# Performance work log

Hardware: AMD Instinct MI355X
Metric: run time of the kernel (lower is better)

The kernel has to match this reference:

```python
import jax, jax.numpy as jnp
import numpy as np

EPS = 1e-12  # VERY_SMALL_NUMBER
LN_EPS = 1e-5
N, NFEAT, NHID, A, P, HOPS = 50000, 256, 128, 32, 4, 2


def setup_inputs() -> dict:
    key = jax.random.key(0)
    ks = jax.random.split(key, 16)
    def w(i, shape, scale=0.05):
        return jax.random.normal(ks[i], shape, dtype=jnp.float32) * scale
    return {
        "x": jax.random.normal(ks[0], (N, NFEAT), dtype=jnp.float32),
        # input_mapper: Linear(nfeat,nhid) -> ReLU -> Linear(nhid,nhid)
        "im_w1": w(1, (NFEAT, NHID)), "im_b1": jnp.zeros((NHID,), jnp.float32),
        "im_w2": w(2, (NHID, NHID)),  "im_b2": jnp.zeros((NHID,), jnp.float32),
        # AnchorGraphLearner
        "anchors": w(3, (A, NHID), 1.0),
        "ml_w1": w(4, (P, 2 * NHID, NHID)), "ml_b1": jnp.zeros((P, NHID), jnp.float32),
        "ml_w2": w(5, (P, NHID)),            "ml_b2": jnp.zeros((P,), jnp.float32),
        # AnchorGNNLayer weights (xavier in torch; scaled randn here)
        "enc_w": w(6, (HOPS, NHID, NHID)), "enc_b": jnp.zeros((HOPS, NHID), jnp.float32),
        # LayerNorm
        "ln_g": jnp.ones((NHID,), jnp.float32), "ln_b": jnp.zeros((NHID,), jnp.float32),
        # classifier: Linear -> PReLU(nhid) -> Linear(nhid,2)
        "cls_w1": w(7, (NHID, NHID)), "cls_b1": jnp.zeros((NHID,), jnp.float32),
        "prelu_a": jnp.full((NHID,), 0.25, jnp.float32),
        "cls_w2": w(8, (NHID, 2)),   "cls_b2": jnp.zeros((2,), jnp.float32),
    }


def _forward(x, im_w1, im_b1, im_w2, im_b2, anchors, ml_w1, ml_b1, ml_w2, ml_b2,
             enc_w, enc_b, ln_g, ln_b, cls_w1, cls_b1, prelu_a, cls_w2, cls_b2):
    nhid = im_w2.shape[-1]
    # input_mapper (dropout is identity in eval)
    h = jnp.maximum(x @ im_w1 + im_b1, 0.0) @ im_w2 + im_b2  # [N, nhid]
    x_loc = h

    # --- AnchorGraphLearner: fused form of cat([x_i, a_j]) @ W1 ---
    Wx, Wa = ml_w1[:, :nhid, :], ml_w1[:, nhid:, :]  # each [P, nhid, nhid]
    attn = jnp.zeros((h.shape[0], anchors.shape[0]), h.dtype)
    for p in range(ml_w1.shape[0]):  # small fixed head count
        hx = h @ Wx[p]                               # [N, nhid]
        ha = anchors @ Wa[p]                         # [A, nhid]
        hid = jnp.maximum(hx[:, None, :] + ha[None, :, :] + ml_b1[p], 0.0)  # [N, A, nhid]
        attn = attn + jax.nn.sigmoid(hid @ ml_w2[p] + ml_b2[p])            # [N, A]
    adj = attn / ml_w1.shape[0]  # mean over heads, [N, A]

    # --- AnchorGNNLayer stack (anchor_mp normalized double matmul) ---
    node_norm = adj / jnp.maximum(adj.sum(axis=0, keepdims=True), EPS)     # col-normalized [N, A]
    anchor_norm = adj / jnp.maximum(adj.sum(axis=1, keepdims=True), EPS)   # row-normalized [N, A]
    xc = h
    for i in range(enc_w.shape[0]):
        support = xc @ enc_w[i]                          # [N, nhid]
        agg = node_norm.T @ support                      # [A, nhid]
        xc = jnp.maximum(anchor_norm @ agg + enc_b[i], 0.0)

    # residual + LayerNorm
    z = xc + x_loc
    mu = z.mean(axis=-1, keepdims=True)
    var = ((z - mu) ** 2).mean(axis=-1, keepdims=True)
    z = (z - mu) * jax.lax.rsqrt(var + LN_EPS) * ln_g + ln_b

    def classifier(t):
        t1 = t @ cls_w1 + cls_b1
        t1 = jnp.where(t1 > 0, t1, prelu_a * t1)  # PReLU(nhid)
        return t1 @ cls_w2 + cls_b2

    pred = classifier(z)                 # [N, 2]
    anchor_logits = classifier(anchors)  # [A, 2]
    anchor_vec = anchors[None]           # [1, A, nhid] (matches unsqueeze(0))
    return (pred, z, anchor_vec, anchor_logits)


def reference(x, im_w1, im_b1, im_w2, im_b2, anchors, ml_w1, ml_b1, ml_w2, ml_b2,
              enc_w, enc_b, ln_g, ln_b, cls_w1, cls_b1, prelu_a, cls_w2, cls_b2):
    return _forward(x, im_w1, im_b1, im_w2, im_b2, anchors, ml_w1, ml_b1, ml_w2, ml_b2,
                    enc_w, enc_b, ln_g, ln_b, cls_w1, cls_b1, prelu_a, cls_w2, cls_b2)
```

## Files before the change

### kernel.cpp

```cpp
#include <hip/hip_runtime.h>
#include <math.h>

#define NN 50000
#define FEAT 256
#define HID 128
#define NA 32
#define NP 4
#define TM 64
#define NBLK 782
#define LDA 132
#define EPSS 1e-12f
#define LN_EPS 1e-5f

typedef unsigned short u16;
typedef __attribute__((ext_vector_type(8))) short bf16x8;
typedef __attribute__((ext_vector_type(4))) float f32x4;

#define ADJ_F   0
#define RS_F    1600000
#define CS_F    1650000
#define AGG0_F  1650032
#define AGG1_F  1654128
#define HB_F    1658256
#define FLAG_F  1674640
#define F_END   1674672
#define XC_U   (2 * F_END)
#define SUP_U  (XC_U + NN * HID)
#define PW_U   (SUP_U + NN * HID)
#define PW_TOT 165638
#define WS_NEED_BYTES ((size_t)(PW_U + PW_TOT) * 2ULL)

#define PK_IMW1T  0
#define PK_IMW2T  32768
#define PK_MLW1T  49152
#define PK_ENCWT  114688
#define PK_CLSW1T 147456
#define PK_IMB1   163840
#define PK_IMB2   163968
#define PK_MLW2   164096
#define PK_ENCB   164608
#define PK_LNG    164864
#define PK_LNB    164992
#define PK_CLSB1  165120
#define PK_PRELU  165248
#define PK_CLSW2  165376
#define PK_CLSB2  165632
#define PK_MLB2   165634
#define PK_TOTAL  165638

#define PRED_OFF 0
#define Z_OFF    100000
#define AV_OFF   6500000
#define AL_OFF   6504096
#define OUT_TOT  6504160

__device__ __constant__ int kNel[19] = {
    NN * FEAT, FEAT * HID, HID, HID * HID, HID, NA * HID,
    NP * 2 * HID * HID, NP * HID, NP * HID, NP, 2 * HID * HID, 2 * HID,
    HID, HID, HID * HID, HID, HID, HID * 2, 2};

__device__ __constant__ int tDst[9]  = {PK_IMW1T,PK_IMW2T,PK_MLW1T,PK_MLW1T+16384,
                                        PK_MLW1T+32768,PK_MLW1T+49152,PK_ENCWT,
                                        PK_ENCWT+16384,PK_CLSW1T};
__device__ __constant__ int tSrcT[9] = {1,3,6,6,6,6,10,10,14};
__device__ __constant__ int tBase[9] = {0,0,0,32768,65536,98304,0,16384,0};
#define VSEG_TOT 1798
__device__ __constant__ int vLen[11] = {128,128,512,256,128,128,128,128,256,2,4};
__device__ __constant__ int vDst[11] = {PK_IMB1,PK_IMB2,PK_MLW2,PK_ENCB,PK_LNG,PK_LNB,
                                        PK_CLSB1,PK_PRELU,PK_CLSW2,PK_CLSB2,PK_MLB2};
__device__ __constant__ int vSrcT[11]= {2,4,8,11,12,13,15,16,17,18,9};

struct P19 { const void* q[19]; };

__device__ __forceinline__ float b2f(u16 u) {
    union { float f; unsigned int i; } v; v.i = ((unsigned int)u) << 16; return v.f;
}
__device__ __forceinline__ u16 f2b(float f) {
    union { float f; unsigned int i; } v; v.f = f;
    unsigned int x = v.i;
    x += 0x7fffu + ((x >> 16) & 1u);
    return (u16)(x >> 16);
}
__device__ __forceinline__ float ldf(const void* p, size_t i, int fl) {
    if (fl == 1) return ((const float*)p)[i];
    if (fl == 0) return b2f(((const u16*)p)[i]);
    return 0.f;
}

__global__ __launch_bounds__(256) void k_detect_all(P19 a, int* __restrict__ flags) {
    __shared__ int sHi[256], sE[256], sO[256];
    const int b = blockIdx.x;
    const u16* p = (const u16*)a.q[b];
    const int M = (kNel[b] < 8192) ? kNel[b] : 8192;
    int cHi = 0, cE = 0, cO = 0;
    for (int j = threadIdx.x; j < M; j += 256) {
        const u16 v = p[j];
        if (j & 1) cO += (v != 0);
        else { cE += (v != 0); cHi += (((v >> 7) & 0xFF) >= 200); }
    }
    sHi[threadIdx.x] = cHi; sE[threadIdx.x] = cE; sO[threadIdx.x] = cO;
    __syncthreads();
    for (int s = 128; s > 0; s >>= 1) {
        if (threadIdx.x < (unsigned)s) {
            sHi[threadIdx.x] += sHi[threadIdx.x + s];
            sE[threadIdx.x]  += sE[threadIdx.x + s];
            sO[threadIdx.x]  += sO[threadIdx.x + s];
        }
        __syncthreads();
    }
    if (threadIdx.x == 0) {
        int f;
        if (sE[0] == 0 && sO[0] == 0) f = 2;
        else if (sHi[0] >= 4 || sE[0] == 0) f = 1;
        else f = 0;
        flags[b] = f;
    }
}

__global__ __launch_bounds__(256) void k_convT(P19 a, const int* __restrict__ flags,
                                               u16* __restrict__ pw) {
    const int b = blockIdx.x;
    if (b == 160) {
        for (int idx = threadIdx.x; idx < VSEG_TOT; idx += 256) {
            int off = idx, s = 0;
            while (off >= vLen[s]) { off -= vLen[s]; ++s; }
            const int si = vSrcT[s];
            pw[vDst[s] + off] = f2b(ldf(a.q[si], off, flags[si]));
        }
        return;
    }
    __shared__ float tle[32][33];
    int s, t;
    if (b < 32) { s = 0; t = b; }
    else        { s = 1 + (b - 32) / 16; t = (b - 32) % 16; }
    const int K = (s == 0) ? 256 : 128;
    const int tn = (t & 3) * 32, tk = (t >> 2) * 32;
    const int si = tSrcT[s], fl = flags[si];
    const int c0 = threadIdx.x & 31, q0 = threadIdx.x >> 5;
#pragma unroll
    for (int i = 0; i < 4; ++i) {
        const int kk = q0 + i * 8;
        tle[kk][c0] = ldf(a.q[si],
                          (size_t)tBase[s] + (size_t)(tk + kk) * 128 + tn + c0, fl);
    }
    __syncthreads();
#pragma unroll
    for (int i = 0; i < 4; ++i) {
        const int nn = q0 + i * 8;
        pw[tDst[s] + (size_t)(tn + nn) * K + tk + c0] = f2b(tle[c0][nn]);
    }
}

__device__ __forceinline__ void mfma_64x128(const u16* As, const u16* Bt,
                                            f32x4 acc[8], int lane, int rowBase) {
    const int lr = lane & 15, lq = lane >> 4;
#pragma unroll
    for (int kc = 0; kc < 4; ++kc) {
        bf16x8 a = *(const bf16x8*)(As + (rowBase + lr) * 136 + kc * 32 + lq * 8);
#pragma unroll
        for (int t = 0; t < 8; ++t) {
            bf16x8 b = *(const bf16x8*)(Bt + (t * 16 + lr) * 136 + kc * 32 + lq * 8);
            acc[t] = __builtin_amdgcn_mfma_f32_16x16x32_bf16(a, b, acc[t], 0, 0, 0);
        }
    }
}

__global__ __launch_bounds__(256) void k_gemm2(const void* __restrict__ A,
                                               const u16* __restrict__ pw,
                                               float* __restrict__ outh,
                                               const int* __restrict__ flags) {
    __shared__ __align__(16) u16 As[64 * 136];
    __shared__ __align__(16) u16 Bt[128 * 136];
    const int fA = flags[0];
    const int tid = threadIdx.x;
    const int row0 = blockIdx.x * TM;
    const int lane = tid & 63, wv = tid >> 6, rowBase = wv * 16;
    const int lr = lane & 15, lq = lane >> 4;
    f32x4 acc[8];
    const f32x4 z4 = {0.f, 0.f, 0.f, 0.f};
#pragma unroll
    for (int t = 0; t < 8; ++t) acc[t] = z4;

    for (int kc = 0; kc < 2; ++kc) {
        for (int i = tid; i < 64 * 32; i += 256) {
            const int m = i >> 5, k4 = (i & 31) << 2;
            const int g = row0 + m;
            ushort4 o; o.x = 0; o.y = 0; o.z = 0; o.w = 0;
            if (g < NN) {
                const size_t idx = (size_t)g * FEAT + kc * 128 + k4;
                if (fA == 1) {
                    float4 v = *(const float4*)((const float*)A + idx);
                    o.x = f2b(v.x); o.y = f2b(v.y); o.z = f2b(v.z); o.w = f2b(v.w);
                } else {
                    o = *(const ushort4*)((const u16*)A + idx);
                }
            }
            *(ushort4*)&As[m * 136 + k4] = o;
        }
        for (int i = tid; i < 128 * 32; i += 256) {
            const int n = i >> 5, k4 = (i & 31) << 2;
            *(ushort4*)&Bt[n * 136 + k4] =
                *(const ushort4*)(pw + PK_IMW1T + (size_t)n * FEAT + kc * 128 + k4);
        }
        __syncthreads();
        mfma_64x128(As, Bt, acc, lane, rowBase);
        __syncthreads();
    }
#pragma unroll
    for (int t = 0; t < 8; ++t) {
        const int col = t * 16 + lr;
        const float bv = b2f(pw[PK_IMB1 + col]);
#pragma unroll
        for (int r = 0; r < 4; ++r)
            As[(rowBase + lq * 4 + r) * 136 + col] = f2b(fmaxf(acc[t][r] + bv, 0.f));
    }
    for (int i = tid; i < 128 * 32; i += 256) {
        const int n = i >> 5, k4 = (i & 31) << 2;
        *(ushort4*)&Bt[n * 136 + k4] =
            *(const ushort4*)(pw + PK_IMW2T + (size_t)n * HID + k4);
    }
    __syncthreads();
    f32x4 acc2[8];
#pragma unroll
    for (int t = 0; t < 8; ++t) acc2[t] = z4;
    mfma_64x128(As, Bt, acc2, lane, rowBase);
#pragma unroll
    for (int t = 0; t < 8; ++t) {
        const int col = t * 16 + lr;
        const float bv = b2f(pw[PK_IMB2 + col]);
#pragma unroll
        for (int r = 0; r < 4; ++r) {
            const int g = row0 + rowBase + lq * 4 + r;
            if (g < NN) outh[(size_t)g * HID + col] = acc2[t][r] + bv;
        }
    }
}

__global__ __launch_bounds__(128) void k_pre(const void* __restrict__ anchors,
                                             const void* __restrict__ ml_w1,
                                             const void* __restrict__ ml_b1,
                                             const void* __restrict__ ml_w2,
                                             float* __restrict__ hb,
                                             float* __restrict__ wc,
                                             const int* __restrict__ flags) {
    __shared__ float sa[HID];
    __shared__ float red[128];
    const int fAn = flags[5], fW1 = flags[6], fB1 = flags[7], fW2 = flags[8];
    const int p = blockIdx.x >> 5, a = blockIdx.x & 31, k = threadIdx.x;
    sa[k] = ldf(anchors, a * HID + k, fAn);
    __syncthreads();
    float acc = ldf(ml_b1, p * HID + k, fB1);
    const size_t wbase = ((size_t)p * 2 * HID + HID) * HID + k;
#pragma unroll 4
    for (int j = 0; j < HID; ++j)
        acc += sa[j] * ldf(ml_w1, wbase + (size_t)j * HID, fW1);
    hb[p * (NA * HID) + k * NA + a] = acc;
    red[k] = 0.5f * ldf(ml_w2, p * HID + k, fW2) * acc;
    __syncthreads();
    for (int st = 64; st > 0; st >>= 1) {
        if (k < st) red[k] += red[k + st];
        __syncthreads();
    }
    if (k == 0) wc[p * NA + a] = red[0];
}

__global__ __launch_bounds__(256) void k_anchor(const void* __restrict__ anchors,
                                                const void* __restrict__ cls_w1,
                                                const void* __restrict__ cls_b1,
                                                const void* __restrict__ prelu_a,
                                                const void* __restrict__ cls_w2,
                                                const void* __restrict__ cls_b2,
                                                float* __restrict__ out,
                                                const int* __restrict__ flags) {
    __shared__ float sa[2][HID];
    __shared__ float st1[2][HID];
    const int fAn = flags[5], fW1 = flags[14], fB1 = flags[15];
    const int fPa = flags[16], fW2 = flags[17], fB2 = flags[18];
    const int tid = threadIdx.x;
    const int a0 = blockIdx.x * 2;
    const int half = tid >> 7, k = tid & 127;
    sa[half][k] = ldf(anchors, (a0 + half) * HID + k, fAn);
    __syncthreads();
    float acc = ldf(cls_b1, k, fB1);
#pragma unroll 4
    for (int j = 0; j < HID; ++j) acc += sa[half][j] * ldf(cls_w1, j * HID + k, fW1);
    const float pa = ldf(prelu_a, k, fPa);
    st1[half][k] = acc > 0.f ? acc : pa * acc;
    __syncthreads();
    if (tid < 4) {
        const int aa = tid >> 1, c = tid & 1;
        float s = ldf(cls_b2, c, fB2);
        for (int j = 0; j < HID; ++j) s += st1[aa][j] * ldf(cls_w2, j * 2 + c, fW2);
        out[AL_OFF + (a0 + aa) * 2 + c] = s;
    }
    if (blockIdx.x == 0) {
        for (int i = tid; i < NA * HID; i += 256)
            out[AV_OFF + i] = ldf(anchors, i, fAn);
    }
}

__global__ __launch_bounds__(256) void k_fattn(const float* __restrict__ h,
                                               const u16* __restrict__ pw,
                                               const float* __restrict__ hb,
                                               const float* __restrict__ wc,
                                               float* __restrict__ adj,
                                               float* __restrict__ rowsum,
                                               float* __restrict__ csPart,
                                               float* __restrict__ part) {
    __shared__ __align__(16) u16 Bt[128 * 136];
    __shared__ float hws[HID];
    __shared__ float wcs[NA];
    __shared__ float swr[4][NA];
    float* hbf = (float*)&Bt[64 * 136];
    const int tid = threadIdx.x;
    const int row0 = blockIdx.x * TM;
    const int lane = tid & 63, wv = tid >> 6, rowBase = wv * 16;
    const int lr = lane & 15, lq = lane >> 4;
    const int g = tid & 3, myrow = tid >> 2;
    const int a0 = g * 8;

    bf16x8 afr[4];
    {
        const int gr = row0 + rowBase + lr;
#pragma unroll
        for (int kc = 0; kc < 4; ++kc) {
            bf16x8 t;
            if (gr < NN) {
                const float* src = h + (size_t)gr * HID + kc * 32 + lq * 8;
                float4 v0 = *(const float4*)src;
                float4 v1 = *(const float4*)(src + 4);
                t[0] = (short)f2b(v0.x); t[1] = (short)f2b(v0.y);
                t[2] = (short)f2b(v0.z); t[3] = (short)f2b(v0.w);
                t[4] = (short)f2b(v1.x); t[5] = (short)f2b(v1.y);
                t[6] = (short)f2b(v1.z); t[7] = (short)f2b(v1.w);
            } else {
#pragma unroll
                for (int j = 0; j < 8; ++j) t[j] = 0;
            }
            afr[kc] = t;
        }
    }

    float adjacc[8];
#pragma unroll
    for (int j = 0; j < 8; ++j) adjacc[j] = 0.f;

    for (int p = 0; p < NP; ++p) {
        __syncthreads();
        for (int i = tid; i < 128 * 32; i += 256) {
            const int n = i >> 5, k4 = (i & 31) << 2;
            *(ushort4*)&Bt[n * 136 + k4] =
                *(const ushort4*)(pw + PK_MLW1T + p * 16384 + n * 128 + k4);
        }
        if (tid < HID) hws[tid] = 0.5f * b2f(pw[PK_MLW2 + p * HID + tid]);
        if (tid < NA) wcs[tid] = wc[p * NA + tid];
        __syncthreads();

        f32x4 acc[8];
        const f32x4 z4 = {0.f, 0.f, 0.f, 0.f};
#pragma unroll
        for (int t = 0; t < 8; ++t) acc[t] = z4;
#pragma unroll
        for (int kc = 0; kc < 4; ++kc)
#pragma unroll
            for (int t = 0; t < 8; ++t) {
                bf16x8 b = *(const bf16x8*)(Bt + (t * 16 + lr) * 136 + kc * 32 + lq * 8);
                acc[t] = __builtin_amdgcn_mfma_f32_16x16x32_bf16(afr[kc], b, acc[t], 0, 0, 0);
            }
        __syncthreads();
#pragma unroll
        for (int t = 0; t < 8; ++t)
#pragma unroll
            for (int r = 0; r < 4; ++r)
                Bt[(rowBase + lq * 4 + r) * 136 + t * 16 + lr] = f2b(acc[t][r]);
        {
            const float4* hbp4 = (const float4*)(hb + (size_t)p * (NA * HID));
#pragma unroll
            for (int j = 0; j < 4; ++j)
                ((float4*)hbf)[tid + j * 256] = hbp4[tid + j * 256];
        }
        __syncthreads();

        const float b2v = b2f(pw[PK_MLB2 + p]);
        float sabs[8], wh = 0.f;
#pragma unroll
        for (int j = 0; j < 8; ++j) sabs[j] = 0.f;

#pragma unroll 4
        for (int kp = 0; kp < 64; ++kp) {
            const unsigned hx2 = *(const unsigned*)&Bt[myrow * 136 + kp * 2];
            union { unsigned u; float f; } u0, u1;
            u0.u = hx2 << 16;
            u1.u = hx2 & 0xffff0000u;
            const float f0 = u0.f, f1 = u1.f;
            const float2 hw2 = *(const float2*)&hws[kp * 2];
            wh = fmaf(hw2.x, f0, wh);
            wh = fmaf(hw2.y, f1, wh);
            const float4 c00 = *(const float4*)&hbf[(kp * 2) * NA + a0];
            const float4 c01 = *(const float4*)&hbf[(kp * 2) * NA + a0 + 4];
            const float4 c10 = *(const float4*)&hbf[(kp * 2 + 1) * NA + a0];
            const float4 c11 = *(const float4*)&hbf[(kp * 2 + 1) * NA + a0 + 4];
            sabs[0] = fmaf(hw2.x, fabsf(f0 + c00.x), sabs[0]);
            sabs[1] = fmaf(hw2.x, fabsf(f0 + c00.y), sabs[1]);
            sabs[2] = fmaf(hw2.x, fabsf(f0 + c00.z), sabs[2]);
            sabs[3] = fmaf(hw2.x, fabsf(f0 + c00.w), sabs[3]);
            sabs[4] = fmaf(hw2.x, fabsf(f0 + c01.x), sabs[4]);
            sabs[5] = fmaf(hw2.x, fabsf(f0 + c01.y), sabs[5]);
            sabs[6] = fmaf(hw2.x, fabsf(f0 + c01.z), sabs[6]);
            sabs[7] = fmaf(hw2.x, fabsf(f0 + c01.w), sabs[7]);
            sabs[0] = fmaf(hw2.y, fabsf(f1 + c10.x), sabs[0]);
            sabs[1] = fmaf(hw2.y, fabsf(f1 + c10.y), sabs[1]);
            sabs[2] = fmaf(hw2.y, fabsf(f1 + c10.z), sabs[2]);
            sabs[3] = fmaf(hw2.y, fabsf(f1 + c10.w), sabs[3]);
            sabs[4] = fmaf(hw2.y, fabsf(f1 + c11.x), sabs[4]);
            sabs[5] = fmaf(hw2.y, fabsf(f1 + c11.y), sabs[5]);
            sabs[6] = fmaf(hw2.y, fabsf(f1 + c11.z), sabs[6]);
            sabs[7] = fmaf(hw2.y, fabsf(f1 + c11.w), sabs[7]);
        }
#pragma unroll
        for (int j = 0; j < 8; ++j) {
            const float s = wh + wcs[a0 + j] + b2v + sabs[j];
            adjacc[j] += 0.25f / (1.f + __expf(-s));
        }
    }

    const int grow = row0 + myrow;
    if (grow >= NN) {
#pragma unroll
        for (int j = 0; j < 8; ++j) adjacc[j] = 0.f;
    }
    if (grow < NN) {
        float* dst = adj + (size_t)grow * NA + a0;
        *(float4*)dst = make_float4(adjacc[0], adjacc[1], adjacc[2], adjacc[3]);
        *(float4*)(dst + 4) = make_float4(adjacc[4], adjacc[5], adjacc[6], adjacc[7]);
    }
    float rs = 0.f;
#pragma unroll
    for (int j = 0; j < 8; ++j) rs += adjacc[j];
    rs += __shfl_xor(rs, 1);
    rs += __shfl_xor(rs, 2);
    if (g == 0 && grow < NN) rowsum[grow] = rs;
    __syncthreads();
#pragma unroll
    for (int kc = 0; kc < 4; ++kc)
        *(bf16x8*)&Bt[(rowBase + lr) * 136 + kc * 32 + lq * 8] = afr[kc];
    float* adjTe = (float*)&Bt[64 * 136];
#pragma unroll
    for (int j = 0; j < 8; ++j)
        adjTe[myrow * 33 + a0 + j] = adjacc[j];
#pragma unroll
    for (int st = 4; st <= 32; st <<= 1)
#pragma unroll
        for (int j = 0; j < 8; ++j) adjacc[j] += __shfl_xor(adjacc[j], st);
    if (lane < 4) {
#pragma unroll
        for (int j = 0; j < 8; ++j) swr[wv][lane * 8 + j] = adjacc[j];
    }
    __syncthreads();
    if (tid < NA)
        csPart[tid * NBLK + blockIdx.x] =
            swr[0][tid] + swr[1][tid] + swr[2][tid] + swr[3][tid];
    const int aA = (tid & 15) * 2, kA = (tid >> 4) * 8;
    float acc2[2][8];
#pragma unroll
    for (int ia = 0; ia < 2; ++ia)
#pragma unroll
        for (int j = 0; j < 8; ++j) acc2[ia][j] = 0.f;
#pragma unroll 4
    for (int n = 0; n < TM; ++n) {
        const float a0v = adjTe[n * 33 + aA], a1v = adjTe[n * 33 + aA + 1];
        ushort4 u0 = *(const ushort4*)&Bt[n * 136 + kA];
        ushort4 u1 = *(const ushort4*)&Bt[n * 136 + kA + 4];
        float sv[8] = {b2f(u0.x), b2f(u0.y), b2f(u0.z), b2f(u0.w),
                       b2f(u1.x), b2f(u1.y), b2f(u1.z), b2f(u1.w)};
#pragma unroll
        for (int j = 0; j < 8; ++j) {
            acc2[0][j] += a0v * sv[j];
            acc2[1][j] += a1v * sv[j];
        }
    }
    float* pdst = part + (size_t)blockIdx.x * (NA * HID);
#pragma unroll
    for (int ia = 0; ia < 2; ++ia) {
        *(float4*)&pdst[(aA + ia) * HID + kA] =
            make_float4(acc2[ia][0], acc2[ia][1], acc2[ia][2], acc2[ia][3]);
        *(float4*)&pdst[(aA + ia) * HID + kA + 4] =
            make_float4(acc2[ia][4], acc2[ia][5], acc2[ia][6], acc2[ia][7]);
    }
}

template<int WCS>
__global__ __launch_bounds__(256) void k_Tred(const float* __restrict__ part,
                                              float* __restrict__ T,
                                              const float* __restrict__ csPart,
                                              float* __restrict__ colsum) {
    __shared__ float red[256];
    const int tid = threadIdx.x;
    if (WCS && blockIdx.x >= 256) {
        const int a = blockIdx.x - 256;
        float s = 0.f;
        for (int b = tid; b < NBLK; b += 256) s += csPart[a * NBLK + b];
        red[tid] = s;
        __syncthreads();
        for (int st = 128; st > 0; st >>= 1) {
            if (tid < st) red[tid] += red[tid + st];
            __syncthreads();
        }
        if (tid == 0) colsum[a] = red[0];
        return;
    }
    const int jj = tid & 15, bq = tid >> 4;
    const int j = blockIdx.x * 16 + jj;
    float s = 0.f;
#pragma unroll 8
    for (int b = bq; b < NBLK; b += 16) s += part[(size_t)b * (NA * HID) + j];
    red[tid] = s;
    __syncthreads();
    if (bq == 0) {
        float t = 0.f;
#pragma unroll
        for (int q = 0; q < 16; ++q) t += red[q * 16 + jj];
        T[j] = t;
    }
}

__global__ __launch_bounds__(128) void k_small(const float* __restrict__ T,
                                               const u16* __restrict__ pw,
                                               const int hop,
                                               float* __restrict__ agg) {
    __shared__ float tr[HID];
    const int a = blockIdx.x, n = threadIdx.x;
    tr[n] = T[a * HID + n];
    __syncthreads();
    const u16* w = pw + PK_ENCWT + hop * HID * HID + n * HID;
    float s = 0.f;
#pragma unroll 4
    for (int j4 = 0; j4 < HID; j4 += 4) {
        ushort4 u = *(const ushort4*)(w + j4);
        s += tr[j4] * b2f(u.x) + tr[j4 + 1] * b2f(u.y) +
             tr[j4 + 2] * b2f(u.z) + tr[j4 + 3] * b2f(u.w);
    }
    agg[a * HID + n] = s;
}

__global__ __launch_bounds__(256) void k_e2a(const float* __restrict__ adj,
                                             const float* __restrict__ rowsum,
                                             const float* __restrict__ colsum,
                                             const float* __restrict__ agg,
                                             const u16* __restrict__ pw,
                                             float* __restrict__ part) {
    __shared__ float aggn[NA][LDA];
    __shared__ float adjT[TM][NA + 1];
    __shared__ __align__(8) u16 xcs[TM * 136];
    __shared__ float csl[NA], rsl[TM];
    const int tid = threadIdx.x;
    const int row0 = blockIdx.x * TM;
    const int n0 = (tid & 31) * 4, m0 = (tid >> 5) * 8;
    const int a0 = (tid & 15) * 2, k0 = (tid >> 4) * 8;

    if (tid < NA) csl[tid] = fmaxf(colsum[tid], EPSS);
    if (tid >= 64 && tid < 128) {
        const int m = tid - 64, g = row0 + m;
        rsl[m] = (g < NN) ? 1.f / fmaxf(rowsum[g], EPSS) : 0.f;
    }
    for (int i = tid; i < TM * NA; i += 256) {
        const int m = i >> 5, a = i & 31, g = row0 + m;
        adjT[m][a] = (g < NN) ? adj[(size_t)g * NA + a] : 0.f;
    }
    __syncthreads();
    for (int i = tid; i < (NA * HID) / 4; i += 256) {
        const int a = i >> 5, k4 = (i & 31) << 2;
        float4 v = *(const float4*)(agg + a * HID + k4);
        const float inv = 1.f / csl[a];
        v.x *= inv; v.y *= inv; v.z *= inv; v.w *= inv;
        *(float4*)&aggn[a][k4] = v;
    }
    float bv[4];
#pragma unroll
    for (int j = 0; j < 4; ++j) bv[j] = b2f(pw[PK_ENCB + n0 + j]);
    __syncthreads();
    float acc[8][4];
#pragma unroll
    for (int i = 0; i < 8; ++i)
#pragma unroll
        for (int j = 0; j < 4; ++j) acc[i][j] = 0.f;
    for (int a = 0; a < NA; ++a) {
        float4 gv = *(const float4*)&aggn[a][n0];
        float gvv[4] = {gv.x, gv.y, gv.z, gv.w};
#pragma unroll
        for (int i = 0; i < 8; ++i) {
            const float av = adjT[m0 + i][a];
#pragma unroll
            for (int j = 0; j < 4; ++j) acc[i][j] += av * gvv[j];
        }
    }
#pragma unroll
    for (int i = 0; i < 8; ++i) {
        const float r = rsl[m0 + i];
        ushort4 o;
        o.x = f2b(fmaxf(r * acc[i][0] + bv[0], 0.f));
        o.y = f2b(fmaxf(r * acc[i][1] + bv[1], 0.f));
        o.z = f2b(fmaxf(r * acc[i][2] + bv[2], 0.f));
        o.w = f2b(fmaxf(r * acc[i][3] + bv[3], 0.f));
        *(ushort4*)&xcs[(m0 + i) * 136 + n0] = o;
    }
    __syncthreads();
    float acc2[2][8];
#pragma unroll
    for (int ia = 0; ia < 2; ++ia)
#pragma unroll
        for (int j = 0; j < 8; ++j) acc2[ia][j] = 0.f;
#pragma unroll 4
    for (int n = 0; n < TM; ++n) {
        const float a0v = adjT[n][a0], a1v = adjT[n][a0 + 1];
        ushort4 u0 = *(const ushort4*)&xcs[n * 136 + k0];
        ushort4 u1 = *(const ushort4*)&xcs[n * 136 + k0 + 4];
        float sv[8] = {b2f(u0.x), b2f(u0.y), b2f(u0.z), b2f(u0.w),
                       b2f(u1.x), b2f(u1.y), b2f(u1.z), b2f(u1.w)};
#pragma unroll
        for (int j = 0; j < 8; ++j) {
            acc2[0][j] += a0v * sv[j];
            acc2[1][j] += a1v * sv[j];
        }
    }
    float* dst = part + (size_t)blockIdx.x * (NA * HID);
#pragma unroll
    for (int ia = 0; ia < 2; ++ia) {
        *(float4*)&dst[(a0 + ia) * HID + k0] =
            make_float4(acc2[ia][0], acc2[ia][1], acc2[ia][2], acc2[ia][3]);
        *(float4*)&dst[(a0 + ia) * HID + k0 + 4] =
            make_float4(acc2[ia][4], acc2[ia][5], acc2[ia][6], acc2[ia][7]);
    }
}

__global__ __launch_bounds__(256) void k_e2f(const float* __restrict__ adj,
                                             const float* __restrict__ rowsum,
                                             const float* __restrict__ colsum,
                                             const float* __restrict__ agg,
                                             const u16* __restrict__ pw,
                                             float* __restrict__ out) {
    __shared__ __align__(16) u16 As[64 * 136];
    __shared__ __align__(16) u16 uniB[128 * 136];
    __shared__ float smu[TM], sinv[TM], sg[HID], sb[HID], w2s[2 * HID];
    __shared__ float csl[NA], rsl[TM];
    float* aggn  = (float*)As;
    float* adjTf = (float*)uniB;
    float* zT    = (float*)uniB;
    const int tid = threadIdx.x;
    const int row0 = blockIdx.x * TM;
    const int lane = tid & 63, wv = tid >> 6, rowBase = wv * 16;
    const int lr = lane & 15, lq = lane >> 4;
    const int n0 = (tid & 31) * 4, m0 = (tid >> 5) * 8;
    const float* h = out + Z_OFF;

    if (tid < NA) csl[tid] = fmaxf(colsum[tid], EPSS);
    if (tid >= 64 && tid < 128) {
        const int m = tid - 64, g = row0 + m;
        rsl[m] = (g < NN) ? 1.f / fmaxf(rowsum[g], EPSS) : 0.f;
    }
    for (int i = tid; i < TM * NA; i += 256) {
        const int m = i >> 5, a = i & 31, g = row0 + m;
        adjTf[m * (NA + 1) + a] = (g < NN) ? adj[(size_t)g * NA + a] : 0.f;
    }
    __syncthreads();
    for (int i = tid; i < (NA * HID) / 4; i += 256) {
        const int a = i >> 5, k4 = (i & 31) << 2;
        float4 v = *(const float4*)(agg + a * HID + k4);
        const float inv = 1.f / csl[a];
        v.x *= inv; v.y *= inv; v.z *= inv; v.w *= inv;
        *(float4*)&aggn[a * LDA + k4] = v;
    }
    __syncthreads();
    float acc[8][4];
#pragma unroll
    for (int i = 0; i < 8; ++i)
#pragma unroll
        for (int j = 0; j < 4; ++j) acc[i][j] = 0.f;
    for (int a = 0; a < NA; ++a) {
        float4 gv = *(const float4*)&aggn[a * LDA + n0];
        float gvv[4] = {gv.x, gv.y, gv.z, gv.w};
#pragma unroll
        for (int i = 0; i < 8; ++i) {
            const float av = adjTf[(m0 + i) * (NA + 1) + a];
#pragma unroll
            for (int j = 0; j < 4; ++j) acc[i][j] += av * gvv[j];
        }
    }
    float bv[4];
#pragma unroll
    for (int j = 0; j < 4; ++j) bv[j] = b2f(pw[PK_ENCB + HID + n0 + j]);
    float xcv[8][4];
#pragma unroll
    for (int i = 0; i < 8; ++i) {
        const float r = rsl[m0 + i];
#pragma unroll
        for (int j = 0; j < 4; ++j)
            xcv[i][j] = fmaxf(r * acc[i][j] + bv[j], 0.f);
    }
    __syncthreads();
#pragma unroll
    for (int i = 0; i < 8; ++i) {
        const int g = row0 + m0 + i;
        float4 hv = make_float4(0.f, 0.f, 0.f, 0.f);
        if (g < NN) hv = *(const float4*)(h + (size_t)g * HID + n0);
        float4 zv = make_float4(xcv[i][0] + hv.x, xcv[i][1] + hv.y,
                                xcv[i][2] + hv.z, xcv[i][3] + hv.w);
        *(float4*)&zT[(m0 + i) * 132 + n0] = zv;
    }
    if (tid < HID) { sg[tid] = b2f(pw[PK_LNG + tid]); sb[tid] = b2f(pw[PK_LNB + tid]); }
    w2s[tid] = b2f(pw[PK_CLSW2 + tid]);
    __syncthreads();
    if (tid < TM) {
        float s = 0.f;
        for (int k = 0; k < HID; ++k) s += zT[tid * 132 + k];
        const float mu = s * (1.f / HID);
        float v = 0.f;
        for (int k = 0; k < HID; ++k) { const float d = zT[tid * 132 + k] - mu; v += d * d; }
        smu[tid] = mu;
        sinv[tid] = rsqrtf(v * (1.f / HID) + LN_EPS);
    }
    __syncthreads();
    for (int i = tid; i < TM * 32; i += 256) {
        const int m = i >> 5, k4 = (i & 31) << 2, g = row0 + m;
        float4 v = *(const float4*)&zT[m * 132 + k4];
        const float mu = smu[m], inv = sinv[m];
        v.x = (v.x - mu) * inv * sg[k4 + 0] + sb[k4 + 0];
        v.y = (v.y - mu) * inv * sg[k4 + 1] + sb[k4 + 1];
        v.z = (v.z - mu) * inv * sg[k4 + 2] + sb[k4 + 2];
        v.w = (v.w - mu) * inv * sg[k4 + 3] + sb[k4 + 3];
        if (g < NN) *(float4*)&out[Z_OFF + (size_t)g * HID + k4] = v;
        ushort4 o; o.x = f2b(v.x); o.y = f2b(v.y); o.z = f2b(v.z); o.w = f2b(v.w);
        *(ushort4*)&As[m * 136 + k4] = o;
    }
    __syncthreads();
    for (int i = tid; i < 128 * 32; i += 256) {
        const int n = i >> 5, k4 = (i & 31) << 2;
        *(ushort4*)&uniB[n * 136 + k4] =
            *(const ushort4*)(pw + PK_CLSW1T + n * 128 + k4);
    }
    __syncthreads();
    f32x4 macc[8];
    const f32x4 z4 = {0.f, 0.f, 0.f, 0.f};
#pragma unroll
    for (int t = 0; t < 8; ++t) macc[t] = z4;
    mfma_64x128(As, uniB, macc, lane, rowBase);
    __syncthreads();
#pragma unroll
    for (int t = 0; t < 8; ++t) {
        const int col = t * 16 + lr;
        const float bc = b2f(pw[PK_CLSB1 + col]);
        const float pa = b2f(pw[PK_PRELU + col]);
#pragma unroll
        for (int r = 0; r < 4; ++r) {
            float v = macc[t][r] + bc;
            v = v > 0.f ? v : pa * v;
            As[(rowBase + lq * 4 + r) * 136 + col] = f2b(v);
        }
    }
    __syncthreads();
    if (tid < 128) {
        const int r = tid >> 1, c = tid & 1, g = row0 + r;
        if (g < NN) {
            float s = b2f(pw[PK_CLSB2 + c]);
            for (int k = 0; k < HID; ++k) s += b2f(As[r * 136 + k]) * w2s[k * 2 + c];
            out[PRED_OFF + (size_t)g * 2 + c] = s;
        }
    }
}

extern "C" void kernel_launch(void* const* d_in, const int* in_sizes, int n_in,
                              void* d_out, int out_size, void* d_ws, size_t ws_size,
                              hipStream_t stream) {
    const bool ok = (n_in >= 19) && (out_size == OUT_TOT) &&
                    (ws_size >= WS_NEED_BYTES) &&
                    (in_sizes[0] == NN * FEAT) && (in_sizes[6] == NP * 2 * HID * HID) &&
                    (in_sizes[10] == 2 * HID * HID) && (in_sizes[17] == HID * 2);
    if (!ok) {
        hipMemsetAsync(d_out, 0, (size_t)OUT_TOT * 4, stream);
        return;
    }

    float* ws    = (float*)d_ws;
    u16*   wsu   = (u16*)d_ws;
    float* out   = (float*)d_out;
    int*   flags = (int*)(ws + FLAG_F);
    float* hbuf  = out + Z_OFF;
    u16*   pw    = wsu + PW_U;
    float* xcf   = (float*)(wsu + XC_U);
    float* csPart = xcf;
    float* partb = xcf + 32768;
    float* Tbuf  = ws + HB_F;
    float* wcv   = ws + AGG1_F;

    P19 pa;
    for (int i = 0; i < 19; ++i) pa.q[i] = d_in[i];
    k_detect_all<<<19, 256, 0, stream>>>(pa, flags);
    k_convT<<<161, 256, 0, stream>>>(pa, flags, pw);

    k_pre<<<NP * NA, 128, 0, stream>>>(d_in[5], d_in[6], d_in[7], d_in[8],
                                       ws + HB_F, wcv, flags);
    k_anchor<<<NA / 2, 256, 0, stream>>>(d_in[5], d_in[14], d_in[15], d_in[16],
                                         d_in[17], d_in[18], out, flags);

    k_gemm2<<<NBLK, 256, 0, stream>>>(d_in[0], pw, hbuf, flags);

    k_fattn<<<NBLK, 256, 0, stream>>>(hbuf, pw, ws + HB_F, wcv, ws + ADJ_F,
                                      ws + RS_F, csPart, partb);

    k_Tred<1><<<288, 256, 0, stream>>>(partb, Tbuf, csPart, ws + CS_F);
    k_small<<<NA, 128, 0, stream>>>(Tbuf, pw, 0, ws + AGG0_F);
    k_e2a<<<NBLK, 256, 0, stream>>>(ws + ADJ_F, ws + RS_F, ws + CS_F, ws + AGG0_F,
                                    pw, partb);
    k_Tred<0><<<256, 256, 0, stream>>>(partb, Tbuf, csPart, ws + CS_F);
    k_small<<<NA, 128, 0, stream>>>(Tbuf, pw, 1, ws + AGG1_F);
    k_e2f<<<NBLK, 256, 0, stream>>>(ws + ADJ_F, ws + RS_F, ws + CS_F, ws + AGG1_F,
                                    pw, out);
}
```

Before: 417.8 us.

## Load input-mapper A operand directly into registers and halve B shared tile

The first GEMM of the input mapper now loads each wave's A fragments for the full 256-wide K dimension straight from global memory into registers, skipping the shared-memory staging of the x tile. The weight tile in shared memory is cut from 128 to 64 output columns and streamed in two halves for both GEMMs. The aim is less LDS traffic and a smaller LDS footprint so more blocks fit per CU. The cost is more registers per thread, extra barriers, and global A loads that are less coalesced.

```diff
diff --git a/kernel.cpp b/kernel.cpp
--- a/kernel.cpp
+++ b/kernel.cpp
@@ -170,41 +170,64 @@
                                                float* __restrict__ outh,
                                                const int* __restrict__ flags) {
     __shared__ __align__(16) u16 As[64 * 136];
-    __shared__ __align__(16) u16 Bt[128 * 136];
+    __shared__ __align__(16) u16 Bt[64 * 136];
     const int fA = flags[0];
     const int tid = threadIdx.x;
     const int row0 = blockIdx.x * TM;
     const int lane = tid & 63, wv = tid >> 6, rowBase = wv * 16;
     const int lr = lane & 15, lq = lane >> 4;
+
+    bf16x8 ax[8];
+    {
+        const int gr = row0 + rowBase + lr;
+#pragma unroll
+        for (int kc = 0; kc < 8; ++kc) {
+            bf16x8 t;
+            if (gr < NN) {
+                const size_t idx = (size_t)gr * FEAT + kc * 32 + lq * 8;
+                if (fA == 1) {
+                    const float* src = (const float*)A + idx;
+                    float4 v0 = *(const float4*)src;
+                    float4 v1 = *(const float4*)(src + 4);
+                    t[0] = (short)f2b(v0.x); t[1] = (short)f2b(v0.y);
+                    t[2] = (short)f2b(v0.z); t[3] = (short)f2b(v0.w);
+                    t[4] = (short)f2b(v1.x); t[5] = (short)f2b(v1.y);
+                    t[6] = (short)f2b(v1.z); t[7] = (short)f2b(v1.w);
+                } else {
+                    t = *(const bf16x8*)((const u16*)A + idx);
+                }
+            } else {
+#pragma unroll
+                for (int j = 0; j < 8; ++j) t[j] = 0;
+            }
+            ax[kc] = t;
+        }
+    }
+
     f32x4 acc[8];
     const f32x4 z4 = {0.f, 0.f, 0.f, 0.f};
 #pragma unroll
     for (int t = 0; t < 8; ++t) acc[t] = z4;
 
-    for (int kc = 0; kc < 2; ++kc) {
-        for (int i = tid; i < 64 * 32; i += 256) {
-            const int m = i >> 5, k4 = (i & 31) << 2;
-            const int g = row0 + m;
-            ushort4 o; o.x = 0; o.y = 0; o.z = 0; o.w = 0;
-            if (g < NN) {
-                const size_t idx = (size_t)g * FEAT + kc * 128 + k4;
-                if (fA == 1) {
-                    float4 v = *(const float4*)((const float*)A + idx);
-                    o.x = f2b(v.x); o.y = f2b(v.y); o.z = f2b(v.z); o.w = f2b(v.w);
-                } else {
-                    o = *(const ushort4*)((const u16*)A + idx);
+    for (int half = 0; half < 2; ++half) {
+        for (int kc2 = 0; kc2 < 2; ++kc2) {
+            __syncthreads();
+            for (int i = tid; i < 64 * 32; i += 256) {
+                const int n = i >> 5, k4 = (i & 31) << 2;
+                *(ushort4*)&Bt[n * 136 + k4] =
+                    *(const ushort4*)(pw + PK_IMW1T +
+                                      (size_t)(half * 64 + n) * FEAT + kc2 * 128 + k4);
+            }
+            __syncthreads();
+#pragma unroll
+            for (int kc = 0; kc < 4; ++kc)
+#pragma unroll
+                for (int tt = 0; tt < 4; ++tt) {
+                    bf16x8 b = *(const bf16x8*)(Bt + (tt * 16 + lr) * 136 + kc * 32 + lq * 8);
+                    acc[half * 4 + tt] = __builtin_amdgcn_mfma_f32_16x16x32_bf16(
+                        ax[kc2 * 4 + kc], b, acc[half * 4 + tt], 0, 0, 0);
                 }
-            }
-            *(ushort4*)&As[m * 136 + k4] = o;
-        }
-        for (int i = tid; i < 128 * 32; i += 256) {
-            const int n = i >> 5, k4 = (i & 31) << 2;
-            *(ushort4*)&Bt[n * 136 + k4] =
-                *(const ushort4*)(pw + PK_IMW1T + (size_t)n * FEAT + kc * 128 + k4);
-        }
-        __syncthreads();
-        mfma_64x128(As, Bt, acc, lane, rowBase);
-        __syncthreads();
+        }
     }
 #pragma unroll
     for (int t = 0; t < 8; ++t) {
@@ -214,16 +237,28 @@
         for (int r = 0; r < 4; ++r)
             As[(rowBase + lq * 4 + r) * 136 + col] = f2b(fmaxf(acc[t][r] + bv, 0.f));
     }
-    for (int i = tid; i < 128 * 32; i += 256) {
-        const int n = i >> 5, k4 = (i & 31) << 2;
-        *(ushort4*)&Bt[n * 136 + k4] =
-            *(const ushort4*)(pw + PK_IMW2T + (size_t)n * HID + k4);
-    }
-    __syncthreads();
     f32x4 acc2[8];
 #pragma unroll
     for (int t = 0; t < 8; ++t) acc2[t] = z4;
-    mfma_64x128(As, Bt, acc2, lane, rowBase);
+    for (int half = 0; half < 2; ++half) {
+        __syncthreads();
+        for (int i = tid; i < 64 * 32; i += 256) {
+            const int n = i >> 5, k4 = (i & 31) << 2;
+            *(ushort4*)&Bt[n * 136 + k4] =
+                *(const ushort4*)(pw + PK_IMW2T + (size_t)(half * 64 + n) * HID + k4);
+        }
+        __syncthreads();
+#pragma unroll
+        for (int kc = 0; kc < 4; ++kc) {
+            bf16x8 a = *(const bf16x8*)(As + (rowBase + lr) * 136 + kc * 32 + lq * 8);
+#pragma unroll
+            for (int tt = 0; tt < 4; ++tt) {
+                bf16x8 b = *(const bf16x8*)(Bt + (tt * 16 + lr) * 136 + kc * 32 + lq * 8);
+                acc2[half * 4 + tt] = __builtin_amdgcn_mfma_f32_16x16x32_bf16(
+                    a, b, acc2[half * 4 + tt], 0, 0, 0);
+            }
+        }
+    }
 #pragma unroll
     for (int t = 0; t < 8; ++t) {
         const int col = t * 16 + lr;
```

Result: faster. 403.9 us (median of 2 runs) (-3.3%).
